# Optimization experiments

Hardware: AMD Instinct MI355X
Metric: run time of the kernel (lower is better)

## Reference

```python
import jax, jax.numpy as jnp
import numpy as np

B, S, F_DIM, H = 2, 2048, 1024, 16
DH = F_DIM // H  # 64


def setup_inputs() -> dict:
    key = jax.random.key(0)
    ks = jax.random.split(key, 12)
    scale = 1.0 / np.sqrt(F_DIM)
    inp = {
        "Q": jax.random.normal(ks[0], (B, S, F_DIM), jnp.float32),
        "K": jax.random.normal(ks[1], (B, S, F_DIM), jnp.float32),
        "V": jax.random.normal(ks[2], (B, S, F_DIM), jnp.float32),
        "mask": jnp.zeros((1, 1, S, S), jnp.float32),
        "Wq": jax.random.uniform(ks[3], (F_DIM, F_DIM), jnp.float32, -scale, scale),
        "bq": jax.random.uniform(ks[4], (F_DIM,), jnp.float32, -scale, scale),
        "Wk": jax.random.uniform(ks[5], (F_DIM, F_DIM), jnp.float32, -scale, scale),
        "bk": jax.random.uniform(ks[6], (F_DIM,), jnp.float32, -scale, scale),
        "Wv": jax.random.uniform(ks[7], (F_DIM, F_DIM), jnp.float32, -scale, scale),
        "bv": jax.random.uniform(ks[8], (F_DIM,), jnp.float32, -scale, scale),
        "Wo": jax.random.uniform(ks[9], (F_DIM, F_DIM), jnp.float32, -scale, scale),
        "bo": jax.random.uniform(ks[10], (F_DIM,), jnp.float32, -scale, scale),
    }
    return inp


def _split_heads(x):
    # [B, S, F] -> [B, H, S, DH]
    b, s, _ = x.shape
    return x.reshape(b, s, H, DH).transpose(0, 2, 1, 3)


def reference(Q, K, V, mask, Wq, bq, Wk, bk, Wv, bv, Wo, bo):
    q = _split_heads(Q @ Wq.T + bq)  # [B, H, S, DH]
    k = _split_heads(K @ Wk.T + bk)
    v = _split_heads(V @ Vv_fix(Wv).T + bv) if False else _split_heads(V @ Wv.T + bv)
    scores = jnp.einsum("bhqd,bhkd->bhqk", q, k) / jnp.sqrt(jnp.float32(DH))
    scores = scores + mask
    probs = jax.nn.softmax(scores, axis=-1)
    attn = jnp.einsum("bhqk,bhkd->bhqd", probs, v)  # [B, H, S, DH]
    out = attn.transpose(0, 2, 1, 3).reshape(Q.shape[0], Q.shape[1], F_DIM)
    return out @ Wo.T + bo
```

## Files before the change

### kernel.cpp

```cpp
#include <hip/hip_runtime.h>
#include <hip/hip_bf16.h>

typedef unsigned short u16;
typedef unsigned int u32;
typedef __attribute__((ext_vector_type(2))) float f32x2;
typedef __attribute__((ext_vector_type(4))) float f32x4;
typedef __attribute__((ext_vector_type(16))) float f32x16;
typedef __attribute__((ext_vector_type(8))) short short8;
typedef __attribute__((ext_vector_type(4))) u32 u32x4;

#define SEQ 2048
#define FD  1024
#define NH  16
#define DHD 64


__device__ __forceinline__ u16 f2bf(float f) {
  __hip_bfloat16 h = __float2bfloat16(f);
  return *reinterpret_cast<u16*>(&h);
}
__device__ __forceinline__ u32 pack2bf(float lo, float hi) {
  return (u32)f2bf(lo) | ((u32)f2bf(hi) << 16);
}
__device__ __forceinline__ u32 cvtpk(float lo, float hi) {
  u32 r;
  asm("v_cvt_pk_bf16_f32 %0, %1, %2" : "=v"(r) : "v"(lo), "v"(hi));
  return r;
}

#define GLOAD_LDS16(gp, lp)                                        \
  __builtin_amdgcn_global_load_lds(                                \
      (const __attribute__((address_space(1))) unsigned int*)(gp), \
      (__attribute__((address_space(3))) unsigned int*)(lp), 16, 0, 0)

__global__ __launch_bounds__(256) void prep_kernel(
    const float* __restrict__ Q, const float* __restrict__ K, const float* __restrict__ V,
    const float* __restrict__ Wq, const float* __restrict__ Wk, const float* __restrict__ Wv,
    const float* __restrict__ Wo,
    u16* __restrict__ Abf, u16* __restrict__ Wbf) {
  const size_t i = ((size_t)blockIdx.x * 256 + threadIdx.x) * 8;
  const float* src;
  u16* dst;
  if (i < 12582912) {
    const int s = (int)(i >> 22);
    const size_t off = i & 0x3FFFFF;
    src = (s == 0 ? Q : s == 1 ? K : V) + off;
    dst = Abf + i;
  } else {
    const size_t j = i - 12582912;
    const int w = (int)(j >> 20);
    const size_t off = j & 0xFFFFF;
    src = (w == 0 ? Wq : w == 1 ? Wk : w == 2 ? Wv : Wo) + off;
    dst = Wbf + j;
  }
  f32x4 a = *reinterpret_cast<const f32x4*>(src);
  f32x4 b = *reinterpret_cast<const f32x4*>(src + 4);
  union { u32 u[4]; short8 s; } pk;
  pk.u[0] = pack2bf(a[0], a[1]); pk.u[1] = pack2bf(a[2], a[3]);
  pk.u[2] = pack2bf(b[0], b[1]); pk.u[3] = pack2bf(b[2], b[3]);
  *reinterpret_cast<short8*>(dst) = pk.s;
}

__device__ __forceinline__ void gemm128_bf16(const u16* __restrict__ A, const u16* __restrict__ W,
                                             int m0, int n0, u16* As, u16* Bs,
                                             f32x4 (&acc)[4][4]) {
  const int tid = threadIdx.x, lane = tid & 63, wv = tid >> 6;
  const int wr = (tid >> 7) & 1, wc = (tid >> 6) & 1;
  const int lr = lane & 15, lk = (lane >> 4) << 3;
  const int srow = lane >> 2;
  const int scol = (lane & 3) << 3;
#pragma unroll
  for (int m = 0; m < 4; ++m)
#pragma unroll
    for (int n = 0; n < 4; ++n) acc[m][n] = {0.f, 0.f, 0.f, 0.f};

  for (int k0 = 0; k0 < FD; k0 += 32) {
    __syncthreads();
#pragma unroll
    for (int c = 0; c < 2; ++c) {
      GLOAD_LDS16(&A[(size_t)(m0 + c * 64 + wv * 16 + srow) * FD + k0 + scol],
                  &As[(c * 64 + wv * 16) * 32]);
      GLOAD_LDS16(&W[(size_t)(n0 + c * 64 + wv * 16 + srow) * FD + k0 + scol],
                  &Bs[(c * 64 + wv * 16) * 32]);
    }
    __syncthreads();
    short8 a[4], b[4];
#pragma unroll
    for (int m = 0; m < 4; ++m)
      a[m] = *reinterpret_cast<const short8*>(&As[(wr * 64 + m * 16 + lr) * 32 + lk]);
#pragma unroll
    for (int n = 0; n < 4; ++n)
      b[n] = *reinterpret_cast<const short8*>(&Bs[(wc * 64 + n * 16 + lr) * 32 + lk]);
#pragma unroll
    for (int m = 0; m < 4; ++m)
#pragma unroll
      for (int n = 0; n < 4; ++n)
        acc[m][n] = __builtin_amdgcn_mfma_f32_16x16x32_bf16(a[m], b[n], acc[m][n], 0, 0, 0);
  }
}

__global__ __launch_bounds__(256) void proj_qkv_kernel(
    const u16* __restrict__ Abf, const u16* __restrict__ Wbf,
    const float* __restrict__ bq, const float* __restrict__ bk, const float* __restrict__ bv,
    const u32* __restrict__ mask_u32, u32* __restrict__ mflag,
    u16* __restrict__ qh, u16* __restrict__ kh, u16* __restrict__ vF) {
  __shared__ u16 As[128 * 32];
  __shared__ u16 Bs[128 * 32];
  const int bid = blockIdx.x;
  if (bid >= 768) {
    const size_t cb = (size_t)(bid - 768) * 2048 + ((size_t)threadIdx.x << 3);
    u32x4 a = *reinterpret_cast<const u32x4*>(&mask_u32[cb]);
    u32x4 b = *reinterpret_cast<const u32x4*>(&mask_u32[cb + 4]);
    u32 o = a[0] | a[1] | a[2] | a[3] | b[0] | b[1] | b[2] | b[3];
    if (__ballot(o != 0) != 0ull && (threadIdx.x & 63) == 0) atomicOr(mflag, 1u);
    return;
  }
  const int which = bid >> 8;
  const int rr = bid & 255;
  const int slot = rr >> 3;
  const int y = (rr & 7) + 8 * (slot & 3);
  const int x = slot >> 2;
  const int m0 = y * 128, n0 = x * 128;
  const u16* A = Abf + ((size_t)which << 22);
  const u16* W = Wbf + ((size_t)which << 20);
  const float* bias = (which == 0) ? bq : (which == 1) ? bk : bv;
  const float qscale = 0.18033688011112042f;

  f32x4 acc[4][4];
  gemm128_bf16(A, W, m0, n0, As, Bs, acc);

  u16* out = (which == 0) ? qh : (which == 1) ? kh : vF;
  const int lane = threadIdx.x & 63;
  const int wr = (threadIdx.x >> 7) & 1, wc = (threadIdx.x >> 6) & 1;
  const int rbase = m0 + wr * 64 + ((lane >> 4) << 2);
  const int cbase = n0 + wc * 64 + (lane & 15);
#pragma unroll
  for (int n = 0; n < 4; ++n) {
    const int col = cbase + n * 16;
    const float bvv = bias[col];
    const int h = col >> 6, dh = col & 63;
#pragma unroll
    for (int m = 0; m < 4; ++m) {
#pragma unroll
      for (int r = 0; r < 4; ++r) {
        const int row = rbase + m * 16 + r;
        const int b = row >> 11, s = row & 2047;
        float v = acc[m][n][r] + bvv;
        if (which == 0) v *= qscale;
        const size_t bhbase = (size_t)(b * 16 + h) * SEQ * DHD;
        size_t idx;
        if (which == 0) {
          idx = bhbase + (size_t)s * 64 + dh;
        } else if (which == 1) {
          idx = bhbase + ((size_t)(((s >> 5) * 4 + (dh >> 4)) * 64
                          + ((dh >> 3) & 1) * 32 + (s & 31)) << 3) + (dh & 7);
        } else {
          idx = bhbase + ((size_t)(((s >> 4) * 2 + (dh >> 5)) * 64
                          + ((s >> 3) & 1) * 32 + (dh & 31)) << 3) + (s & 7);
        }
        out[idx] = f2bf(v);
      }
    }
  }
}

__device__ __forceinline__ void load_ktile(const u16* __restrict__ kp, int kv0, int lane,
                                           short8 (&kf)[8]) {
#pragma unroll
  for (int h2 = 0; h2 < 2; ++h2)
#pragma unroll
    for (int d = 0; d < 4; ++d)
      kf[h2 * 4 + d] = *reinterpret_cast<const short8*>(
          &kp[((size_t)((((kv0 >> 5) + h2) * 4 + d) * 64 + lane)) << 3]);
}

#define PV(i) pp[(i) >> 1][(i) & 1]

__device__ __forceinline__ void attn_tile(
    const short8 (&kf)[8], const u16* __restrict__ vp, const float* __restrict__ mrow,
    u32 has_mask, int kv0, int lane, int hi, const short8 (&qf)[4],
    f32x16 (&oacc)[2], float& m2, float& lsum) {
  const float L2E = 1.44269504088896340736f;
  short8 vf[8];
#pragma unroll
  for (int kb = 0; kb < 4; ++kb)
#pragma unroll
    for (int db = 0; db < 2; ++db)
      vf[kb * 2 + db] = *reinterpret_cast<const short8*>(
          &vp[((size_t)((((kv0 >> 4) + kb) * 2 + db) * 64 + lane)) << 3]);

  f32x16 st[2];
  __builtin_amdgcn_s_setprio(1);
#pragma unroll
  for (int h2 = 0; h2 < 2; ++h2) {
    f32x16 z;
#pragma unroll
    for (int e = 0; e < 16; ++e) z[e] = 0.f;
#pragma unroll
    for (int d = 0; d < 4; ++d)
      z = __builtin_amdgcn_mfma_f32_32x32x16_bf16(kf[h2 * 4 + d], qf[d], z, 0, 0, 0);
    st[h2] = z;
  }
  __builtin_amdgcn_s_setprio(0);
  f32x2 pp[16];
  if (__builtin_expect(has_mask != 0, 0)) {
#pragma unroll
    for (int h2 = 0; h2 < 2; ++h2)
#pragma unroll
      for (int g = 0; g < 4; ++g) {
        f32x4 mv = *reinterpret_cast<const f32x4*>(&mrow[kv0 + h2 * 32 + g * 8 + hi * 4]);
        const int pb = h2 * 8 + g * 2;
        f32x2 m0 = {mv[0], mv[1]}, m1 = {mv[2], mv[3]};
        f32x2 s0 = {st[h2][g * 4 + 0], st[h2][g * 4 + 1]};
        f32x2 s1 = {st[h2][g * 4 + 2], st[h2][g * 4 + 3]};
        pp[pb]     = m0 * L2E + s0;
        pp[pb + 1] = m1 * L2E + s1;
      }
  } else {
#pragma unroll
    for (int j = 0; j < 16; ++j)
      pp[j] = {st[j >> 3][(2 * j) & 15], st[j >> 3][(2 * j + 1) & 15]};
  }
  float t[11];
#pragma unroll
  for (int i = 0; i < 10; ++i)
    t[i] = fmaxf(fmaxf(PV(3 * i), PV(3 * i + 1)), PV(3 * i + 2));
  t[10] = fmaxf(PV(30), PV(31));
  const float u0 = fmaxf(fmaxf(t[0], t[1]), t[2]);
  const float u1 = fmaxf(fmaxf(t[3], t[4]), t[5]);
  const float u2 = fmaxf(fmaxf(t[6], t[7]), t[8]);
  const float u3 = fmaxf(t[9], t[10]);
  float mt = fmaxf(fmaxf(u0, u1), fmaxf(u2, u3));
  mt = fmaxf(mt, __shfl_xor(mt, 32));
  if (!__all(mt - m2 <= 8.f)) {
    const float mnew = fmaxf(m2, mt);
    const float alpha = __builtin_amdgcn_exp2f(m2 - mnew);
    m2 = mnew;
    lsum *= alpha;
#pragma unroll
    for (int e = 0; e < 16; ++e) { oacc[0][e] *= alpha; oacc[1][e] *= alpha; }
  }
  const f32x2 mm = {m2, m2};
#pragma unroll
  for (int j = 0; j < 16; ++j) pp[j] -= mm;
#pragma unroll
  for (int j = 0; j < 16; ++j) {
    pp[j][0] = __builtin_amdgcn_exp2f(pp[j][0]);
    pp[j][1] = __builtin_amdgcn_exp2f(pp[j][1]);
  }
  f32x2 sa[8];
#pragma unroll
  for (int j = 0; j < 8; ++j) sa[j] = pp[j] + pp[j + 8];
  f32x2 sb[4];
#pragma unroll
  for (int j = 0; j < 4; ++j) sb[j] = sa[j] + sa[j + 4];
  f32x2 sc0 = sb[0] + sb[2], sc1 = sb[1] + sb[3];
  f32x2 sd = sc0 + sc1;
  float ssum = sd[0] + sd[1];
  ssum += __shfl_xor(ssum, 32);
  lsum += ssum;

  __builtin_amdgcn_s_setprio(1);
#pragma unroll
  for (int kb = 0; kb < 4; ++kb) {
    const int pb = (kb >> 1) * 16 + (kb & 1) * 8;
    u32 x = cvtpk(PV(pb + 0), PV(pb + 1));
    u32 y = cvtpk(PV(pb + 4), PV(pb + 5));
    asm volatile("v_permlane32_swap_b32 %0, %1" : "+v"(x), "+v"(y));
    u32 zz = cvtpk(PV(pb + 2), PV(pb + 3));
    u32 w = cvtpk(PV(pb + 6), PV(pb + 7));
    asm volatile("v_permlane32_swap_b32 %0, %1" : "+v"(zz), "+v"(w));
    union { u32 u[4]; short8 s; } bf;
    bf.u[0] = x; bf.u[1] = zz; bf.u[2] = y; bf.u[3] = w;
#pragma unroll
    for (int db = 0; db < 2; ++db)
      oacc[db] = __builtin_amdgcn_mfma_f32_32x32x16_bf16(vf[kb * 2 + db], bf.s, oacc[db], 0, 0, 0);
  }
  __builtin_amdgcn_s_setprio(0);
}

__global__ __launch_bounds__(256, 2) void attn_kernel(
    const u16* __restrict__ qh, const u16* __restrict__ kh, const u16* __restrict__ vF,
    const float* __restrict__ mask, const u32* __restrict__ mflag, u16* __restrict__ O) {
  __shared__ float red[2][2][2][32];
  __shared__ float osum[2][32][68];
  const int wave = threadIdx.x >> 6, lane = threadIdx.x & 63;
  const int qgrp = wave >> 1, half = wave & 1;
  const int bid = blockIdx.x;
  const int vid = (bid & 7) * 128 + (bid >> 3);
  const int bh = vid >> 5;
  const int q0 = (vid & 31) * 64 + qgrp * 32;
  const int lq = lane & 31;
  const int hi = lane >> 5;
  const u16* qp = qh + (size_t)bh * SEQ * DHD;
  const u16* kp = kh + (size_t)bh * SEQ * DHD;
  const u16* vp = vF + (size_t)bh * SEQ * DHD;
  const float* mrow = mask + (size_t)(q0 + lq) * SEQ;
  const u32 has_mask = *mflag;

  short8 qf[4];
#pragma unroll
  for (int d = 0; d < 4; ++d)
    qf[d] = *reinterpret_cast<const short8*>(&qp[(size_t)(q0 + lq) * DHD + d * 16 + hi * 8]);

  f32x16 oacc[2];
#pragma unroll
  for (int e = 0; e < 16; ++e) { oacc[0][e] = 0.f; oacc[1][e] = 0.f; }
  float m2 = -INFINITY, lsum = 0.f;

  const int kvb = half * (SEQ / 2);
  short8 ka[8], kb2[8];
  load_ktile(kp, kvb, lane, ka);
  for (int it = 0; it < 16; it += 2) {
    const int kv0 = kvb + (it << 6);
    load_ktile(kp, kv0 + 64, lane, kb2);
    attn_tile(ka, vp, mrow, has_mask, kv0, lane, hi, qf, oacc, m2, lsum);
    load_ktile(kp, (it == 14) ? kvb : kv0 + 128, lane, ka);
    attn_tile(kb2, vp, mrow, has_mask, kv0 + 64, lane, hi, qf, oacc, m2, lsum);
  }

  if (hi == 0) { red[qgrp][half][0][lq] = m2; red[qgrp][half][1][lq] = lsum; }
  __syncthreads();
  const float Mfin = fmaxf(red[qgrp][0][0][lq], red[qgrp][1][0][lq]);
  const float beta = __builtin_amdgcn_exp2f(m2 - Mfin);
  const float mo = red[qgrp][half ^ 1][0][lq];
  const float lo = red[qgrp][half ^ 1][1][lq];
  const float ltot = lsum * beta + lo * __builtin_amdgcn_exp2f(mo - Mfin);
#pragma unroll
  for (int e = 0; e < 16; ++e) { oacc[0][e] *= beta; oacc[1][e] *= beta; }
  if (half == 0) {
#pragma unroll
    for (int db = 0; db < 2; ++db)
#pragma unroll
      for (int g = 0; g < 4; ++g) {
        f32x4 v = {oacc[db][g * 4], oacc[db][g * 4 + 1], oacc[db][g * 4 + 2], oacc[db][g * 4 + 3]};
        *reinterpret_cast<f32x4*>(&osum[qgrp][lq][db * 32 + g * 8 + hi * 4]) = v;
      }
  }
  __syncthreads();
  if (half == 1) {
    const int b = bh >> 4, h = bh & 15;
    const float inv = 1.0f / ltot;
    u16* orow = O + ((size_t)(b * SEQ + q0 + lq) * NH + h) * DHD;
#pragma unroll
    for (int db = 0; db < 2; ++db)
#pragma unroll
      for (int g = 0; g < 4; ++g) {
        f32x4 s = *reinterpret_cast<const f32x4*>(&osum[qgrp][lq][db * 32 + g * 8 + hi * 4]);
        union { u32 u[2]; unsigned long long ll; } pk;
        pk.u[0] = cvtpk((s[0] + oacc[db][g * 4 + 0]) * inv, (s[1] + oacc[db][g * 4 + 1]) * inv);
        pk.u[1] = cvtpk((s[2] + oacc[db][g * 4 + 2]) * inv, (s[3] + oacc[db][g * 4 + 3]) * inv);
        *reinterpret_cast<unsigned long long*>(&orow[db * 32 + g * 8 + hi * 4]) = pk.ll;
      }
  }
}

__global__ __launch_bounds__(256) void out_proj_kernel(
    const u16* __restrict__ O, const u16* __restrict__ WoB, const float* __restrict__ bo,
    float* __restrict__ out) {
  __shared__ u16 As[128 * 32];
  __shared__ u16 Bs[128 * 32];
  const int rr = blockIdx.x;
  const int slot = rr >> 3;
  const int y = (rr & 7) + 8 * (slot & 3);
  const int x = slot >> 2;
  const int m0 = y * 128, n0 = x * 128;
  f32x4 acc[4][4];
  gemm128_bf16(O, WoB, m0, n0, As, Bs, acc);

  const int lane = threadIdx.x & 63;
  const int wr = (threadIdx.x >> 7) & 1, wc = (threadIdx.x >> 6) & 1;
  const int rbase = m0 + wr * 64 + ((lane >> 4) << 2);
  const int cbase = n0 + wc * 64 + (lane & 15);
#pragma unroll
  for (int n = 0; n < 4; ++n) {
    const int col = cbase + n * 16;
    const float bvv = bo[col];
#pragma unroll
    for (int m = 0; m < 4; ++m)
#pragma unroll
      for (int r = 0; r < 4; ++r) {
        const int row = rbase + m * 16 + r;
        out[(size_t)row * FD + col] = acc[m][n][r] + bvv;
      }
  }
}

extern "C" void kernel_launch(void* const* d_in, const int* in_sizes, int n_in,
                              void* d_out, int out_size, void* d_ws, size_t ws_size,
                              hipStream_t stream) {
  (void)in_sizes; (void)n_in; (void)out_size; (void)ws_size;
  const float* Q    = (const float*)d_in[0];
  const float* K    = (const float*)d_in[1];
  const float* V    = (const float*)d_in[2];
  const float* mask = (const float*)d_in[3];
  const float* Wq   = (const float*)d_in[4];
  const float* bq   = (const float*)d_in[5];
  const float* Wk   = (const float*)d_in[6];
  const float* bk   = (const float*)d_in[7];
  const float* Wv   = (const float*)d_in[8];
  const float* bv   = (const float*)d_in[9];
  const float* Wo   = (const float*)d_in[10];
  const float* bo   = (const float*)d_in[11];
  float* out = (float*)d_out;

  u16* ws = (u16*)d_ws;
  const size_t SZ = (size_t)4096 * 1024;
  u16* qh  = ws;
  u16* kh  = qh + SZ;
  u16* vF  = kh + SZ;
  u16* O   = vF + SZ;
  u16* Abf = O + SZ;
  u16* Wbf = Abf + 3 * SZ;
  u32* mflag = (u32*)(Wbf + 4 * (size_t)1024 * 1024);

  hipMemsetAsync(mflag, 0, 4, stream);
  prep_kernel<<<dim3(8192), 256, 0, stream>>>(Q, K, V, Wq, Wk, Wv, Wo, Abf, Wbf);

  proj_qkv_kernel<<<dim3(2816), 256, 0, stream>>>(Abf, Wbf, bq, bk, bv,
                                                  (const u32*)mask, mflag, qh, kh, vF);

  attn_kernel<<<dim3(1024), 256, 0, stream>>>(qh, kh, vF, mask, mflag, O);

  out_proj_kernel<<<dim3(256), 256, 0, stream>>>(O, Wbf + 3 * (size_t)1024 * 1024, bo, out);
}
```

Measured before the change: 137.2 us.

## Fuse fp32-to-bf16 activation conversion into QKV projection GEMM

The prep kernel no longer converts Q/K/V activations to bf16. The QKV projection GEMM now reads fp32 activations directly, converts them in registers with v_cvt_pk_bf16_f32, and writes them to LDS, while weights still stream in through global_load_lds. This removes a full extra write-and-read pass over 12M activation elements and shrinks the workspace. In exchange, each A tile is fetched again by every column block at twice the bytes, and the A loads become synchronous register loads rather than async LDS loads.

```diff
diff --git a/kernel.cpp b/kernel.cpp
--- a/kernel.cpp
+++ b/kernel.cpp
@@ -34,25 +34,13 @@
       (__attribute__((address_space(3))) unsigned int*)(lp), 16, 0, 0)
 
 __global__ __launch_bounds__(256) void prep_kernel(
-    const float* __restrict__ Q, const float* __restrict__ K, const float* __restrict__ V,
     const float* __restrict__ Wq, const float* __restrict__ Wk, const float* __restrict__ Wv,
-    const float* __restrict__ Wo,
-    u16* __restrict__ Abf, u16* __restrict__ Wbf) {
-  const size_t i = ((size_t)blockIdx.x * 256 + threadIdx.x) * 8;
-  const float* src;
-  u16* dst;
-  if (i < 12582912) {
-    const int s = (int)(i >> 22);
-    const size_t off = i & 0x3FFFFF;
-    src = (s == 0 ? Q : s == 1 ? K : V) + off;
-    dst = Abf + i;
-  } else {
-    const size_t j = i - 12582912;
-    const int w = (int)(j >> 20);
-    const size_t off = j & 0xFFFFF;
-    src = (w == 0 ? Wq : w == 1 ? Wk : w == 2 ? Wv : Wo) + off;
-    dst = Wbf + j;
-  }
+    const float* __restrict__ Wo, u16* __restrict__ Wbf) {
+  const size_t j = ((size_t)blockIdx.x * 256 + threadIdx.x) * 8;
+  const int w = (int)(j >> 20);
+  const size_t off = j & 0xFFFFF;
+  const float* src = (w == 0 ? Wq : w == 1 ? Wk : w == 2 ? Wv : Wo) + off;
+  u16* dst = Wbf + j;
   f32x4 a = *reinterpret_cast<const f32x4*>(src);
   f32x4 b = *reinterpret_cast<const f32x4*>(src + 4);
   union { u32 u[4]; short8 s; } pk;
@@ -99,8 +87,59 @@
   }
 }
 
+__device__ __forceinline__ void gemm128_mixed(const float* __restrict__ A,
+                                              const u16* __restrict__ W,
+                                              int m0, int n0, u16* As, u16* Bs,
+                                              f32x4 (&acc)[4][4]) {
+  const int tid = threadIdx.x, lane = tid & 63, wv = tid >> 6;
+  const int wr = (tid >> 7) & 1, wc = (tid >> 6) & 1;
+  const int lr = lane & 15, lk = (lane >> 4) << 3;
+  const int srow = lane >> 2;
+  const int scol = (lane & 3) << 3;
+#pragma unroll
+  for (int m = 0; m < 4; ++m)
+#pragma unroll
+    for (int n = 0; n < 4; ++n) acc[m][n] = {0.f, 0.f, 0.f, 0.f};
+
+  for (int k0 = 0; k0 < FD; k0 += 32) {
+    __syncthreads();
+#pragma unroll
+    for (int c = 0; c < 2; ++c)
+      GLOAD_LDS16(&W[(size_t)(n0 + c * 64 + wv * 16 + srow) * FD + k0 + scol],
+                  &Bs[(c * 64 + wv * 16) * 32]);
+    f32x4 a0[2], a1[2];
+#pragma unroll
+    for (int c = 0; c < 2; ++c) {
+      const float* s = A + (size_t)(m0 + c * 64 + wv * 16 + srow) * FD + k0 + scol;
+      a0[c] = *reinterpret_cast<const f32x4*>(s);
+      a1[c] = *reinterpret_cast<const f32x4*>(s + 4);
+    }
+#pragma unroll
+    for (int c = 0; c < 2; ++c) {
+      union { u32 u[4]; short8 s8; } pk;
+      pk.u[0] = cvtpk(a0[c][0], a0[c][1]); pk.u[1] = cvtpk(a0[c][2], a0[c][3]);
+      pk.u[2] = cvtpk(a1[c][0], a1[c][1]); pk.u[3] = cvtpk(a1[c][2], a1[c][3]);
+      *reinterpret_cast<short8*>(&As[(c * 64 + wv * 16 + srow) * 32 + scol]) = pk.s8;
+    }
+    __syncthreads();
+    short8 a[4], b[4];
+#pragma unroll
+    for (int m = 0; m < 4; ++m)
+      a[m] = *reinterpret_cast<const short8*>(&As[(wr * 64 + m * 16 + lr) * 32 + lk]);
+#pragma unroll
+    for (int n = 0; n < 4; ++n)
+      b[n] = *reinterpret_cast<const short8*>(&Bs[(wc * 64 + n * 16 + lr) * 32 + lk]);
+#pragma unroll
+    for (int m = 0; m < 4; ++m)
+#pragma unroll
+      for (int n = 0; n < 4; ++n)
+        acc[m][n] = __builtin_amdgcn_mfma_f32_16x16x32_bf16(a[m], b[n], acc[m][n], 0, 0, 0);
+  }
+}
+
 __global__ __launch_bounds__(256) void proj_qkv_kernel(
-    const u16* __restrict__ Abf, const u16* __restrict__ Wbf,
+    const float* __restrict__ Q, const float* __restrict__ K, const float* __restrict__ V,
+    const u16* __restrict__ Wbf,
     const float* __restrict__ bq, const float* __restrict__ bk, const float* __restrict__ bv,
     const u32* __restrict__ mask_u32, u32* __restrict__ mflag,
     u16* __restrict__ qh, u16* __restrict__ kh, u16* __restrict__ vF) {
@@ -121,13 +160,13 @@
   const int y = (rr & 7) + 8 * (slot & 3);
   const int x = slot >> 2;
   const int m0 = y * 128, n0 = x * 128;
-  const u16* A = Abf + ((size_t)which << 22);
+  const float* A = (which == 0) ? Q : (which == 1) ? K : V;
   const u16* W = Wbf + ((size_t)which << 20);
   const float* bias = (which == 0) ? bq : (which == 1) ? bk : bv;
   const float qscale = 0.18033688011112042f;
 
   f32x4 acc[4][4];
-  gemm128_bf16(A, W, m0, n0, As, Bs, acc);
+  gemm128_mixed(A, W, m0, n0, As, Bs, acc);
 
   u16* out = (which == 0) ? qh : (which == 1) ? kh : vF;
   const int lane = threadIdx.x & 63;
@@ -410,14 +449,13 @@
   u16* kh  = qh + SZ;
   u16* vF  = kh + SZ;
   u16* O   = vF + SZ;
-  u16* Abf = O + SZ;
-  u16* Wbf = Abf + 3 * SZ;
+  u16* Wbf = O + SZ;
   u32* mflag = (u32*)(Wbf + 4 * (size_t)1024 * 1024);
 
   hipMemsetAsync(mflag, 0, 4, stream);
-  prep_kernel<<<dim3(8192), 256, 0, stream>>>(Q, K, V, Wq, Wk, Wv, Wo, Abf, Wbf);
-
-  proj_qkv_kernel<<<dim3(2816), 256, 0, stream>>>(Abf, Wbf, bq, bk, bv,
+  prep_kernel<<<dim3(2048), 256, 0, stream>>>(Wq, Wk, Wv, Wo, Wbf);
+
+  proj_qkv_kernel<<<dim3(2816), 256, 0, stream>>>(Q, K, V, Wbf, bq, bk, bv,
                                                   (const u32*)mask, mflag, qh, kh, vF);
 
   attn_kernel<<<dim3(1024), 256, 0, stream>>>(qh, kh, vF, mask, mflag, O);
```

After: 153.2 us. 11.6% more time.
